# Kernel optimization log

Hardware: AMD Instinct MI355X
Metric: run time of the kernel (lower is better)

Reference implementation:

```python
import jax, jax.numpy as jnp
import numpy as np

Q = 10000   # num_question
D = 64      # dim_s
M = 50      # size_m
B = 64      # batch
T = 512     # seq_len


def setup_inputs() -> dict:
    key = jax.random.key(0)
    ks = jax.random.split(key, 14)
    s = 1.0 / np.sqrt(D)
    inp = {
        "question": jax.random.randint(ks[0], (B, T), 0, Q, dtype=jnp.int32),
        "response": jax.random.randint(ks[1], (B, T), 0, 2, dtype=jnp.int32),
        "mask": jnp.ones((B, T), dtype=jnp.float32),
        "k_emb": jax.random.normal(ks[2], (Q, D), jnp.float32) * s,
        "v_emb": jax.random.normal(ks[3], (2 * Q, D), jnp.float32) * s,
        "Mk": jax.random.normal(ks[4], (M, D), jnp.float32) * np.sqrt(2.0 / D),
        "Mv0": jax.random.normal(ks[5], (M, D), jnp.float32) * np.sqrt(2.0 / D),
        "e_W": jax.random.normal(ks[6], (D, D), jnp.float32) * s,
        "e_b": jnp.zeros((D,), jnp.float32),
        "a_W": jax.random.normal(ks[7], (D, D), jnp.float32) * s,
        "a_b": jnp.zeros((D,), jnp.float32),
        "f_W": jax.random.normal(ks[8], (2 * D, D), jnp.float32) * (1.0 / np.sqrt(2 * D)),
        "f_b": jnp.zeros((D,), jnp.float32),
        "p_W": jax.random.normal(ks[9], (D, 1), jnp.float32) * s,
        "p_b": jnp.zeros((1,), jnp.float32),
    }
    return inp


def reference(question, response, mask, k_emb, v_emb, Mk, Mv0,
              e_W, e_b, a_W, a_b, f_W, f_b, p_W, p_b):
    num_q = k_emb.shape[0]
    bsz = question.shape[0]
    x = question + num_q * response                      # [B,T] combined ids
    k = k_emb[question]                                  # [B,T,D]
    v = v_emb[x]                                         # [B,T,D]
    w = jax.nn.softmax(k @ Mk.T, axis=-1)                # [B,T,M] read/write weights
    e = jax.nn.sigmoid(v @ e_W + e_b)                    # [B,T,D] erase
    a = jnp.tanh(v @ a_W + a_b)                          # [B,T,D] add

    def step(Mvt, inp):
        wt, et, at, mt = inp                             # [B,M],[B,D],[B,D],[B]
        Mvn = Mvt * (1.0 - wt[:, :, None] * et[:, None, :]) + wt[:, :, None] * at[:, None, :]
        Mvt = jnp.where(mt[:, None, None] == 1, Mvn, Mvt)
        return Mvt, Mvt

    Mv0b = jnp.broadcast_to(Mv0, (bsz,) + Mv0.shape)     # [B,M,D]
    xs = (jnp.swapaxes(w, 0, 1), jnp.swapaxes(e, 0, 1),
          jnp.swapaxes(a, 0, 1), mask.T)
    _, Mv_seq = jax.lax.scan(step, Mv0b, xs)             # [T,B,M,D] states after steps 0..T-1
    # read at step t (t>=1) uses state after step t-1
    Mv_read = jnp.swapaxes(Mv_seq[:-1], 0, 1)            # [B,T-1,M,D]
    read = jnp.einsum('btm,btmd->btd', w[:, 1:], Mv_read)
    f = jnp.tanh(jnp.concatenate([read, k[:, 1:]], axis=-1) @ f_W + f_b)
    p = (f @ p_W + p_b).squeeze(-1)                      # [B,T-1]
    return p
```

## Files before the change

### kernel.cpp

```cpp
#include <hip/hip_runtime.h>
#include <cstddef>

#define QN 10000
#define DD 64
#define MM 50
#define BB 64
#define TT 512
#define WPAD 52
#define MG 25

__global__ __launch_bounds__(256) void kPre(
    const int* __restrict__ question, const int* __restrict__ response,
    const float* __restrict__ mask,
    const float* __restrict__ k_emb, const float* __restrict__ v_emb,
    const float* __restrict__ Mk,
    const float* __restrict__ e_W, const float* __restrict__ e_b,
    const float* __restrict__ a_W, const float* __restrict__ a_b,
    float* __restrict__ w_buf, float* __restrict__ e_buf,
    float* __restrict__ a_buf) {
  const int lane = (int)(threadIdx.x & 63);
  const int wslot = __builtin_amdgcn_readfirstlane((int)(threadIdx.x >> 6));
  const int gw = blockIdx.x * 4 + wslot;
  const int NW = gridDim.x * 4;
  const int third = NW / 3;
  if (gw >= 3 * third) return;
  const int role = gw / third;
  const int idx = gw - role * third;
  const int stride4 = third * 4;

  if (role == 0) {
    float mk[64];
    const int mrow = lane < MM ? lane : (MM - 1);
#pragma unroll
    for (int i = 0; i < 64; i += 4) {
      const float4 t4 = *(const float4*)(Mk + mrow * 64 + i);
      mk[i] = t4.x; mk[i + 1] = t4.y; mk[i + 2] = t4.z; mk[i + 3] = t4.w;
    }
    for (int base = idx * 4; base < BB * TT; base += stride4) {
      const int4 q4 = *(const int4*)(question + base);
      const float* __restrict__ kr0 = k_emb + (size_t)q4.x * 64;
      const float* __restrict__ kr1 = k_emb + (size_t)q4.y * 64;
      const float* __restrict__ kr2 = k_emb + (size_t)q4.z * 64;
      const float* __restrict__ kr3 = k_emb + (size_t)q4.w * 64;
      float l00=0.f,l01=0.f,l02=0.f,l03=0.f;
      float l10=0.f,l11=0.f,l12=0.f,l13=0.f;
      float l20=0.f,l21=0.f,l22=0.f,l23=0.f;
      float l30=0.f,l31=0.f,l32=0.f,l33=0.f;
#pragma unroll
      for (int i = 0; i < 64; i += 4) {
        const float4 k0 = *(const float4*)(kr0 + i);
        const float4 k1 = *(const float4*)(kr1 + i);
        const float4 k2 = *(const float4*)(kr2 + i);
        const float4 k3 = *(const float4*)(kr3 + i);
        l00 = fmaf(k0.x, mk[i], l00); l01 = fmaf(k0.y, mk[i+1], l01);
        l02 = fmaf(k0.z, mk[i+2], l02); l03 = fmaf(k0.w, mk[i+3], l03);
        l10 = fmaf(k1.x, mk[i], l10); l11 = fmaf(k1.y, mk[i+1], l11);
        l12 = fmaf(k1.z, mk[i+2], l12); l13 = fmaf(k1.w, mk[i+3], l13);
        l20 = fmaf(k2.x, mk[i], l20); l21 = fmaf(k2.y, mk[i+1], l21);
        l22 = fmaf(k2.z, mk[i+2], l22); l23 = fmaf(k2.w, mk[i+3], l23);
        l30 = fmaf(k3.x, mk[i], l30); l31 = fmaf(k3.y, mk[i+1], l31);
        l32 = fmaf(k3.z, mk[i+2], l32); l33 = fmaf(k3.w, mk[i+3], l33);
      }
      float lm[4];
      lm[0] = (l00 + l01) + (l02 + l03);
      lm[1] = (l10 + l11) + (l12 + l13);
      lm[2] = (l20 + l21) + (l22 + l23);
      lm[3] = (l30 + l31) + (l32 + l33);
#pragma unroll
      for (int r = 0; r < 4; ++r) {
        float lv = (lane < MM) ? lm[r] : -3.4e38f;
#pragma unroll
        for (int off = 32; off > 0; off >>= 1) lv = fmaxf(lv, __shfl_xor(lv, off));
        float pe = (lane < MM) ? __expf(lm[r] - lv) : 0.f;
        float ss = pe;
#pragma unroll
        for (int off = 32; off > 0; off >>= 1) ss += __shfl_xor(ss, off);
        if (lane < MM) w_buf[(size_t)(base + r) * WPAD + lane] = pe / ss;
      }
    }
  } else if (role == 1) {
    float ew[64];
#pragma unroll
    for (int i = 0; i < 64; ++i) ew[i] = e_W[i * 64 + lane];
    const float eb = e_b[lane];
    for (int base = idx * 4; base < BB * TT; base += stride4) {
      const int4 q4 = *(const int4*)(question + base);
      const int4 r4 = *(const int4*)(response + base);
      const float4 m4 = *(const float4*)(mask + base);
      const float* __restrict__ v0 = v_emb + ((size_t)q4.x + (size_t)QN * r4.x) * 64;
      const float* __restrict__ v1 = v_emb + ((size_t)q4.y + (size_t)QN * r4.y) * 64;
      const float* __restrict__ v2 = v_emb + ((size_t)q4.z + (size_t)QN * r4.z) * 64;
      const float* __restrict__ v3 = v_emb + ((size_t)q4.w + (size_t)QN * r4.w) * 64;
      float e00 = eb, e01 = 0.f, e10 = eb, e11 = 0.f;
      float e20 = eb, e21 = 0.f, e30 = eb, e31 = 0.f;
#pragma unroll
      for (int i = 0; i < 64; i += 2) {
        const float2 a0 = *(const float2*)(v0 + i);
        const float2 a1 = *(const float2*)(v1 + i);
        const float2 a2 = *(const float2*)(v2 + i);
        const float2 a3 = *(const float2*)(v3 + i);
        e00 = fmaf(a0.x, ew[i], e00); e01 = fmaf(a0.y, ew[i+1], e01);
        e10 = fmaf(a1.x, ew[i], e10); e11 = fmaf(a1.y, ew[i+1], e11);
        e20 = fmaf(a2.x, ew[i], e20); e21 = fmaf(a2.y, ew[i+1], e21);
        e30 = fmaf(a3.x, ew[i], e30); e31 = fmaf(a3.y, ew[i+1], e31);
      }
      const float mf0 = (m4.x == 1.0f) ? 1.0f : 0.0f;
      const float mf1 = (m4.y == 1.0f) ? 1.0f : 0.0f;
      const float mf2 = (m4.z == 1.0f) ? 1.0f : 0.0f;
      const float mf3 = (m4.w == 1.0f) ? 1.0f : 0.0f;
      e_buf[(size_t)(base + 0) * 64 + lane] = mf0 / (1.f + __expf(-(e00 + e01)));
      e_buf[(size_t)(base + 1) * 64 + lane] = mf1 / (1.f + __expf(-(e10 + e11)));
      e_buf[(size_t)(base + 2) * 64 + lane] = mf2 / (1.f + __expf(-(e20 + e21)));
      e_buf[(size_t)(base + 3) * 64 + lane] = mf3 / (1.f + __expf(-(e30 + e31)));
    }
  } else {
    float aw[64];
#pragma unroll
    for (int i = 0; i < 64; ++i) aw[i] = a_W[i * 64 + lane];
    const float ab = a_b[lane];
    for (int base = idx * 4; base < BB * TT; base += stride4) {
      const int4 q4 = *(const int4*)(question + base);
      const int4 r4 = *(const int4*)(response + base);
      const float4 m4 = *(const float4*)(mask + base);
      const float* __restrict__ v0 = v_emb + ((size_t)q4.x + (size_t)QN * r4.x) * 64;
      const float* __restrict__ v1 = v_emb + ((size_t)q4.y + (size_t)QN * r4.y) * 64;
      const float* __restrict__ v2 = v_emb + ((size_t)q4.z + (size_t)QN * r4.z) * 64;
      const float* __restrict__ v3 = v_emb + ((size_t)q4.w + (size_t)QN * r4.w) * 64;
      float a00 = ab, a01 = 0.f, a10 = ab, a11 = 0.f;
      float a20 = ab, a21 = 0.f, a30 = ab, a31 = 0.f;
#pragma unroll
      for (int i = 0; i < 64; i += 2) {
        const float2 x0 = *(const float2*)(v0 + i);
        const float2 x1 = *(const float2*)(v1 + i);
        const float2 x2 = *(const float2*)(v2 + i);
        const float2 x3 = *(const float2*)(v3 + i);
        a00 = fmaf(x0.x, aw[i], a00); a01 = fmaf(x0.y, aw[i+1], a01);
        a10 = fmaf(x1.x, aw[i], a10); a11 = fmaf(x1.y, aw[i+1], a11);
        a20 = fmaf(x2.x, aw[i], a20); a21 = fmaf(x2.y, aw[i+1], a21);
        a30 = fmaf(x3.x, aw[i], a30); a31 = fmaf(x3.y, aw[i+1], a31);
      }
      const float mf0 = (m4.x == 1.0f) ? 1.0f : 0.0f;
      const float mf1 = (m4.y == 1.0f) ? 1.0f : 0.0f;
      const float mf2 = (m4.z == 1.0f) ? 1.0f : 0.0f;
      const float mf3 = (m4.w == 1.0f) ? 1.0f : 0.0f;
      const float s0 = a00 + a01, s1 = a10 + a11, s2 = a20 + a21, s3 = a30 + a31;
      a_buf[(size_t)(base + 0) * 64 + lane] = mf0 * (1.f - 2.f / (__expf(2.f * s0) + 1.f));
      a_buf[(size_t)(base + 1) * 64 + lane] = mf1 * (1.f - 2.f / (__expf(2.f * s1) + 1.f));
      a_buf[(size_t)(base + 2) * 64 + lane] = mf2 * (1.f - 2.f / (__expf(2.f * s2) + 1.f));
      a_buf[(size_t)(base + 3) * 64 + lane] = mf3 * (1.f - 2.f / (__expf(2.f * s3) + 1.f));
    }
  }
}

__global__ __launch_bounds__(256) void kA16(
    const float* __restrict__ w_buf, const float* __restrict__ e_buf,
    const float* __restrict__ a_buf, float* __restrict__ AB) {
  const int lane = (int)(threadIdx.x & 63);
  const int wslot = __builtin_amdgcn_readfirstlane((int)(threadIdx.x >> 6));
  const int u2 = blockIdx.x * 4 + wslot;
  if (u2 >= BB * 32 * 2) return;
  const int g = u2 & 1;
  const int unit = u2 >> 1;
  const int b = unit >> 5;
  const int c = unit & 31;
  const size_t rowbase = (size_t)b * TT + c * 16;
  const size_t eb0 = rowbase * 64 + lane;

  float ev[16], av[16];
#pragma unroll
  for (int j = 0; j < 16; ++j) {
    ev[j] = e_buf[eb0 + (size_t)j * 64];
    av[j] = a_buf[eb0 + (size_t)j * 64];
  }

  float Am[MG], Bm[MG];
#pragma unroll
  for (int m = 0; m < MG; ++m) { Am[m] = 1.f; Bm[m] = 0.f; }

#pragma unroll
  for (int j = 0; j < 16; ++j) {
    const float* __restrict__ wr = w_buf + (rowbase + j) * WPAD + g * MG;
#pragma unroll
    for (int m = 0; m < MG; ++m) {
      const float wm = wr[m];
      const float al = fmaf(-wm, ev[j], 1.0f);
      const float be = wm * av[j];
      Am[m] *= al;
      Bm[m] = fmaf(Bm[m], al, be);
    }
  }
  float* __restrict__ abp = AB + (size_t)unit * 6400 + (g * MG) * 128 + lane * 2;
#pragma unroll
  for (int m = 0; m < MG; ++m) {
    float2 o; o.x = Am[m]; o.y = Bm[m];
    *(float2*)(abp + m * 128) = o;
  }
}

__global__ __launch_bounds__(256) void kB_entry(
    const float* __restrict__ AB, const float* __restrict__ Mv0,
    float* __restrict__ entry, int C) {
  const int NT = gridDim.x * 256;
  for (int idx = blockIdx.x * 256 + (int)threadIdx.x; idx < BB * MM * 64;
       idx += NT) {
    const int b = idx / (MM * 64);
    const int r = idx - b * (MM * 64);
    float s = Mv0[r];
    const float* __restrict__ abp = AB + (size_t)b * C * 6400 + (size_t)r * 2;
    float* __restrict__ ep = entry + (size_t)b * C * 3200 + r;
    if (C == 32) {
      float2 ab[32];
#pragma unroll
      for (int c = 0; c < 32; ++c)
        ab[c] = *(const float2*)(abp + (size_t)c * 6400);
#pragma unroll
      for (int c = 0; c < 32; ++c) {
        ep[(size_t)c * 3200] = s;
        s = fmaf(ab[c].x, s, ab[c].y);
      }
    } else {
      float2 cur = *(const float2*)(abp);
      for (int c = 0; c < C; ++c) {
        ep[(size_t)c * 3200] = s;
        float2 nxt; nxt.x = 1.f; nxt.y = 0.f;
        if (c + 1 < C) nxt = *(const float2*)(abp + (size_t)(c + 1) * 6400);
        s = fmaf(cur.x, s, cur.y);
        cur = nxt;
      }
    }
  }
}

__global__ __launch_bounds__(256) void kC16(
    const float* __restrict__ w_buf, const float* __restrict__ e_buf,
    const float* __restrict__ a_buf, const float* __restrict__ entry,
    float* __restrict__ read2) {
  const int lane = (int)(threadIdx.x & 63);
  const int wslot = __builtin_amdgcn_readfirstlane((int)(threadIdx.x >> 6));
  const int u2 = blockIdx.x * 4 + wslot;
  if (u2 >= BB * 32 * 2) return;
  const int g = u2 & 1;
  const int unit = u2 >> 1;
  const int b = unit >> 5;
  const int c = unit & 31;
  const size_t RN = (size_t)BB * (TT - 1) * 64;
  const size_t rowbase = (size_t)b * TT + c * 16;
  const size_t eb0 = rowbase * 64 + lane;

  float ev[16], av[16];
#pragma unroll
  for (int j = 0; j < 16; ++j) {
    ev[j] = e_buf[eb0 + (size_t)j * 64];
    av[j] = a_buf[eb0 + (size_t)j * 64];
  }

  float s[MG];
  {
    const float* __restrict__ ep =
        entry + (size_t)unit * 3200 + (g * MG) * 64 + lane;
#pragma unroll
    for (int m = 0; m < MG; ++m) s[m] = ep[m * 64];
  }

  const int t0 = c * 16;
  float* __restrict__ rb = read2 + (size_t)g * RN;
#pragma unroll
  for (int j = 0; j < 16; ++j) {
    const int t = t0 + j;
    const float* __restrict__ wr = w_buf + (rowbase + j) * WPAD + g * MG;
    if (t >= 1) {
      float a0 = 0.f, a1 = 0.f;
#pragma unroll
      for (int m = 0; m < MG - 1; m += 2) {
        a0 = fmaf(wr[m], s[m], a0);
        a1 = fmaf(wr[m + 1], s[m + 1], a1);
      }
      a0 = fmaf(wr[MG - 1], s[MG - 1], a0);
      rb[((size_t)b * (TT - 1) + (t - 1)) * 64 + lane] = a0 + a1;
    }
#pragma unroll
    for (int m = 0; m < MG; ++m)
      s[m] = fmaf(wr[m], fmaf(-s[m], ev[j], av[j]), s[m]);
  }
}

__global__ __launch_bounds__(256) void kA_chunk(
    const float* __restrict__ w_buf, const float* __restrict__ e_buf,
    const float* __restrict__ a_buf, float* __restrict__ AB, int logC, int L) {
  const int lane = (int)(threadIdx.x & 63);
  const int wslot = __builtin_amdgcn_readfirstlane((int)(threadIdx.x >> 6));
  const int NW = gridDim.x * 4;
  const int C = 1 << logC;
  for (int u2 = blockIdx.x * 4 + wslot; u2 < BB * C * 2; u2 += NW) {
    const int g = u2 & 1;
    const int unit = u2 >> 1;
    const int b = unit >> logC;
    const int c = unit & (C - 1);
    float Am[MG], Bm[MG];
#pragma unroll
    for (int m = 0; m < MG; ++m) { Am[m] = 1.f; Bm[m] = 0.f; }
    const size_t rowbase = (size_t)b * TT + c * L;
#pragma unroll 2
    for (int j = 0; j < L; ++j) {
      const size_t row = rowbase + j;
      const float ed = e_buf[row * 64 + lane];
      const float ad = a_buf[row * 64 + lane];
      const float* __restrict__ wr = w_buf + row * WPAD + g * MG;
#pragma unroll
      for (int m = 0; m < MG; ++m) {
        const float wm = wr[m];
        const float al = fmaf(-wm, ed, 1.0f);
        const float be = wm * ad;
        Am[m] *= al;
        Bm[m] = fmaf(Bm[m], al, be);
      }
    }
    float* __restrict__ abp = AB + (size_t)unit * 6400 + (g * MG) * 128 + lane * 2;
#pragma unroll
    for (int m = 0; m < MG; ++m) {
      float2 o; o.x = Am[m]; o.y = Bm[m];
      *(float2*)(abp + m * 128) = o;
    }
  }
}

__global__ __launch_bounds__(256) void kC_read(
    const float* __restrict__ w_buf, const float* __restrict__ e_buf,
    const float* __restrict__ a_buf, const float* __restrict__ entry,
    const float* __restrict__ Mv0, float* __restrict__ read2,
    int logC, int L, int use_mv0) {
  const int lane = (int)(threadIdx.x & 63);
  const int wslot = __builtin_amdgcn_readfirstlane((int)(threadIdx.x >> 6));
  const int NW = gridDim.x * 4;
  const int C = 1 << logC;
  const size_t RN = (size_t)BB * (TT - 1) * 64;
  for (int u2 = blockIdx.x * 4 + wslot; u2 < BB * C * 2; u2 += NW) {
    const int g = u2 & 1;
    const int unit = u2 >> 1;
    const int b = unit >> logC;
    const int c = unit & (C - 1);
    float s[MG];
    if (use_mv0) {
#pragma unroll
      for (int m = 0; m < MG; ++m) s[m] = Mv0[(g * MG + m) * 64 + lane];
    } else {
      const float* __restrict__ ep =
          entry + (size_t)unit * 3200 + (g * MG) * 64 + lane;
#pragma unroll
      for (int m = 0; m < MG; ++m) s[m] = ep[m * 64];
    }
    const int t0 = c * L;
    float* __restrict__ rb = read2 + (size_t)g * RN;
    for (int j = 0; j < L; ++j) {
      const int t = t0 + j;
      const size_t row = (size_t)b * TT + t;
      const float ed = e_buf[row * 64 + lane];
      const float ad = a_buf[row * 64 + lane];
      const float* __restrict__ wr = w_buf + row * WPAD + g * MG;
      if (t >= 1) {
        float a0 = 0.f, a1 = 0.f;
#pragma unroll
        for (int m = 0; m < MG - 1; m += 2) {
          a0 = fmaf(wr[m], s[m], a0);
          a1 = fmaf(wr[m + 1], s[m + 1], a1);
        }
        a0 = fmaf(wr[MG - 1], s[MG - 1], a0);
        rb[((size_t)b * (TT - 1) + (t - 1)) * 64 + lane] = a0 + a1;
      }
#pragma unroll
      for (int m = 0; m < MG; ++m)
        s[m] = fmaf(wr[m], fmaf(-s[m], ed, ad), s[m]);
    }
  }
}

__global__ __launch_bounds__(256) void k3_out(
    const int* __restrict__ question, const float* __restrict__ k_emb,
    const float* __restrict__ read2,
    const float* __restrict__ f_W, const float* __restrict__ f_b,
    const float* __restrict__ p_W, const float* __restrict__ p_b,
    float* __restrict__ out) {
  const int lane = (int)(threadIdx.x & 63);
  const int wslot = __builtin_amdgcn_readfirstlane((int)(threadIdx.x >> 6));
  const int NW = gridDim.x * 4;
  const size_t RN = (size_t)BB * (TT - 1) * 64;

  float fw[128];
#pragma unroll
  for (int i = 0; i < 128; ++i) fw[i] = f_W[i * 64 + lane];
  const float fb = f_b[lane];
  const float pw = p_W[lane];
  const float pb = p_b[0];

  for (int row = blockIdx.x * 4 + wslot; row < BB * (TT - 1); row += NW) {
    const int b = row / (TT - 1);
    const int tp = row - b * (TT - 1);
    const float* __restrict__ r0 = read2 + (size_t)row * 64;
    const float* __restrict__ r1 = r0 + RN;
    const int qn = question[b * TT + tp + 1];
    const float* __restrict__ krow = k_emb + (size_t)qn * 64;

    float f0 = fb, f1 = 0.f, f2 = 0.f, f3 = 0.f;
#pragma unroll
    for (int i = 0; i < 64; i += 4) {
      const float4 x0 = *(const float4*)(r0 + i);
      const float4 x1 = *(const float4*)(r1 + i);
      f0 = fmaf(x0.x + x1.x, fw[i], f0);
      f1 = fmaf(x0.y + x1.y, fw[i + 1], f1);
      f2 = fmaf(x0.z + x1.z, fw[i + 2], f2);
      f3 = fmaf(x0.w + x1.w, fw[i + 3], f3);
    }
#pragma unroll
    for (int i = 0; i < 64; i += 4) {
      const float4 kv = *(const float4*)(krow + i);
      f0 = fmaf(kv.x, fw[64 + i], f0);
      f1 = fmaf(kv.y, fw[64 + i + 1], f1);
      f2 = fmaf(kv.z, fw[64 + i + 2], f2);
      f3 = fmaf(kv.w, fw[64 + i + 3], f3);
    }
    const float f = (f0 + f1) + (f2 + f3);
    const float t2 = __expf(2.f * f);
    const float fv = 1.f - 2.f / (t2 + 1.f);
    float acc = fv * pw;
#pragma unroll
    for (int off = 32; off > 0; off >>= 1) acc += __shfl_xor(acc, off);
    if (lane == 0) out[row] = acc + pb;
  }
}

extern "C" void kernel_launch(void* const* d_in, const int* in_sizes, int n_in,
                              void* d_out, int out_size, void* d_ws, size_t ws_size,
                              hipStream_t stream) {
  const int*   question = (const int*)d_in[0];
  const int*   response = (const int*)d_in[1];
  const float* mask     = (const float*)d_in[2];
  const float* k_emb    = (const float*)d_in[3];
  const float* v_emb    = (const float*)d_in[4];
  const float* Mk       = (const float*)d_in[5];
  const float* Mv0      = (const float*)d_in[6];
  const float* e_W      = (const float*)d_in[7];
  const float* e_b      = (const float*)d_in[8];
  const float* a_W      = (const float*)d_in[9];
  const float* a_b      = (const float*)d_in[10];
  const float* f_W      = (const float*)d_in[11];
  const float* f_b      = (const float*)d_in[12];
  const float* p_W      = (const float*)d_in[13];
  const float* p_b      = (const float*)d_in[14];
  float* out = (float*)d_out;

  const size_t wN  = (size_t)BB * TT * WPAD;
  const size_t eN  = (size_t)BB * TT * 64;
  const size_t r2N = 2ull * BB * (TT - 1) * 64;
  float* ws = (float*)d_ws;
  float* w_buf  = ws;
  float* e_buf  = w_buf + wN;
  float* a_buf  = e_buf + eN;
  float* read2  = a_buf + eN;
  float* AB_arr = read2 + r2N;
  const size_t baseN = wN + 2 * eN + r2N;

  int C = 32, logC = 5;
  while (C >= 2) {
    const size_t need = (baseN + 9600ull * BB * C) * sizeof(float);
    if (need <= ws_size) break;
    C >>= 1; logC -= 1;
  }
  int useChunks = (C >= 2);
  if (!useChunks) { C = 1; logC = 0; }
  const int L = TT / C;
  float* entry = AB_arr + 6400ull * BB * C;

  hipLaunchKernelGGL(kPre, dim3(2048), dim3(256), 0, stream,
                     question, response, mask, k_emb, v_emb, Mk,
                     e_W, e_b, a_W, a_b, w_buf, e_buf, a_buf);

  if (C == 32) {
    hipLaunchKernelGGL(kA16, dim3(1024), dim3(256), 0, stream,
                       w_buf, e_buf, a_buf, AB_arr);
    hipLaunchKernelGGL(kB_entry, dim3((BB * MM * 64 + 255) / 256), dim3(256),
                       0, stream, AB_arr, Mv0, entry, C);
    hipLaunchKernelGGL(kC16, dim3(1024), dim3(256), 0, stream,
                       w_buf, e_buf, a_buf, entry, read2);
  } else {
    if (useChunks) {
      const int ublocksA = (BB * C * 2 + 3) / 4;
      hipLaunchKernelGGL(kA_chunk, dim3(ublocksA), dim3(256), 0, stream,
                         w_buf, e_buf, a_buf, AB_arr, logC, L);
      hipLaunchKernelGGL(kB_entry, dim3((BB * MM * 64 + 255) / 256), dim3(256),
                         0, stream, AB_arr, Mv0, entry, C);
    }
    const int ublocksC = (BB * C * 2 + 3) / 4;
    hipLaunchKernelGGL(kC_read, dim3(ublocksC), dim3(256), 0, stream,
                       w_buf, e_buf, a_buf, entry, Mv0, read2,
                       logC, L, useChunks ? 0 : 1);
  }

  hipLaunchKernelGGL(k3_out, dim3(1024), dim3(256), 0, stream,
                     question, k_emb, read2, f_W, f_b, p_W, p_b, out);
}
```

Measured before the change: 211.4 us.

## Fuse preprocessing with chunk scan and read with output projection

Replaces the five-kernel chunked-scan pipeline with three kernels. kPreA computes w/e/a for one 16-step chunk per block and builds the chunk's affine transfer coefficients from LDS. kCD replays each chunk from its entry state and feeds the read vectors straight into the f/p projection through LDS, so the read2 intermediate never goes through global memory. This saves two launches and a large round trip of intermediates, but per-block parallelism drops (192- and 128-thread blocks with heavy register use) and the fallback kPre path was rewritten to one row per wave.

```diff
diff --git a/kernel.cpp b/kernel.cpp
--- a/kernel.cpp
+++ b/kernel.cpp
@@ -8,6 +8,318 @@
 #define TT 512
 #define WPAD 52
 #define MG 25
+
+
+__global__ __attribute__((amdgpu_waves_per_eu(1, 2))) __launch_bounds__(192)
+void kPreA(
+    const int* __restrict__ question, const int* __restrict__ response,
+    const float* __restrict__ mask,
+    const float* __restrict__ k_emb, const float* __restrict__ v_emb,
+    const float* __restrict__ Mk,
+    const float* __restrict__ e_W, const float* __restrict__ e_b,
+    const float* __restrict__ a_W, const float* __restrict__ a_b,
+    float* __restrict__ w_buf, float* __restrict__ e_buf,
+    float* __restrict__ a_buf, float* __restrict__ AB) {
+  __shared__ float w_lds[16][52];
+  __shared__ float e_lds[16][64];
+  __shared__ float a_lds[16][64];
+  const int lane = (int)(threadIdx.x & 63);
+  const int wslot = __builtin_amdgcn_readfirstlane((int)(threadIdx.x >> 6));
+  const int unit = blockIdx.x;
+  const int b = unit >> 5;
+  const int c = unit & 31;
+  const size_t rowbase = (size_t)b * TT + c * 16;
+
+  if (wslot == 0) {
+    float mk[64];
+    const int mrow = lane < MM ? lane : (MM - 1);
+#pragma unroll
+    for (int i = 0; i < 64; i += 4) {
+      const float4 t4 = *(const float4*)(Mk + mrow * 64 + i);
+      mk[i] = t4.x; mk[i + 1] = t4.y; mk[i + 2] = t4.z; mk[i + 3] = t4.w;
+    }
+#pragma unroll
+    for (int base = 0; base < 16; base += 4) {
+      const int4 q4 = *(const int4*)(question + rowbase + base);
+      const float* __restrict__ kr0 = k_emb + (size_t)q4.x * 64;
+      const float* __restrict__ kr1 = k_emb + (size_t)q4.y * 64;
+      const float* __restrict__ kr2 = k_emb + (size_t)q4.z * 64;
+      const float* __restrict__ kr3 = k_emb + (size_t)q4.w * 64;
+      float l00=0.f,l01=0.f,l02=0.f,l03=0.f;
+      float l10=0.f,l11=0.f,l12=0.f,l13=0.f;
+      float l20=0.f,l21=0.f,l22=0.f,l23=0.f;
+      float l30=0.f,l31=0.f,l32=0.f,l33=0.f;
+#pragma unroll
+      for (int i = 0; i < 64; i += 4) {
+        const float4 k0 = *(const float4*)(kr0 + i);
+        const float4 k1 = *(const float4*)(kr1 + i);
+        const float4 k2 = *(const float4*)(kr2 + i);
+        const float4 k3 = *(const float4*)(kr3 + i);
+        l00 = fmaf(k0.x, mk[i], l00); l01 = fmaf(k0.y, mk[i+1], l01);
+        l02 = fmaf(k0.z, mk[i+2], l02); l03 = fmaf(k0.w, mk[i+3], l03);
+        l10 = fmaf(k1.x, mk[i], l10); l11 = fmaf(k1.y, mk[i+1], l11);
+        l12 = fmaf(k1.z, mk[i+2], l12); l13 = fmaf(k1.w, mk[i+3], l13);
+        l20 = fmaf(k2.x, mk[i], l20); l21 = fmaf(k2.y, mk[i+1], l21);
+        l22 = fmaf(k2.z, mk[i+2], l22); l23 = fmaf(k2.w, mk[i+3], l23);
+        l30 = fmaf(k3.x, mk[i], l30); l31 = fmaf(k3.y, mk[i+1], l31);
+        l32 = fmaf(k3.z, mk[i+2], l32); l33 = fmaf(k3.w, mk[i+3], l33);
+      }
+      float lm[4];
+      lm[0] = (l00 + l01) + (l02 + l03);
+      lm[1] = (l10 + l11) + (l12 + l13);
+      lm[2] = (l20 + l21) + (l22 + l23);
+      lm[3] = (l30 + l31) + (l32 + l33);
+#pragma unroll
+      for (int r = 0; r < 4; ++r) {
+        float lv = (lane < MM) ? lm[r] : -3.4e38f;
+#pragma unroll
+        for (int off = 32; off > 0; off >>= 1) lv = fmaxf(lv, __shfl_xor(lv, off));
+        float pe = (lane < MM) ? __expf(lm[r] - lv) : 0.f;
+        float ss = pe;
+#pragma unroll
+        for (int off = 32; off > 0; off >>= 1) ss += __shfl_xor(ss, off);
+        if (lane < MM) {
+          const float wv = pe / ss;
+          w_buf[(rowbase + base + r) * WPAD + lane] = wv;
+          w_lds[base + r][lane] = wv;
+        }
+      }
+    }
+  } else if (wslot == 1) {
+    float ew[64];
+#pragma unroll
+    for (int i = 0; i < 64; ++i) ew[i] = e_W[i * 64 + lane];
+    const float eb = e_b[lane];
+#pragma unroll
+    for (int base = 0; base < 16; base += 4) {
+      const int4 q4 = *(const int4*)(question + rowbase + base);
+      const int4 r4 = *(const int4*)(response + rowbase + base);
+      const float4 m4 = *(const float4*)(mask + rowbase + base);
+      const float* __restrict__ v0 = v_emb + ((size_t)q4.x + (size_t)QN * r4.x) * 64;
+      const float* __restrict__ v1 = v_emb + ((size_t)q4.y + (size_t)QN * r4.y) * 64;
+      const float* __restrict__ v2 = v_emb + ((size_t)q4.z + (size_t)QN * r4.z) * 64;
+      const float* __restrict__ v3 = v_emb + ((size_t)q4.w + (size_t)QN * r4.w) * 64;
+      float e00 = eb, e01 = 0.f, e10 = eb, e11 = 0.f;
+      float e20 = eb, e21 = 0.f, e30 = eb, e31 = 0.f;
+#pragma unroll
+      for (int i = 0; i < 64; i += 2) {
+        const float2 a0 = *(const float2*)(v0 + i);
+        const float2 a1 = *(const float2*)(v1 + i);
+        const float2 a2 = *(const float2*)(v2 + i);
+        const float2 a3 = *(const float2*)(v3 + i);
+        e00 = fmaf(a0.x, ew[i], e00); e01 = fmaf(a0.y, ew[i+1], e01);
+        e10 = fmaf(a1.x, ew[i], e10); e11 = fmaf(a1.y, ew[i+1], e11);
+        e20 = fmaf(a2.x, ew[i], e20); e21 = fmaf(a2.y, ew[i+1], e21);
+        e30 = fmaf(a3.x, ew[i], e30); e31 = fmaf(a3.y, ew[i+1], e31);
+      }
+      const float mf0 = (m4.x == 1.0f) ? 1.0f : 0.0f;
+      const float mf1 = (m4.y == 1.0f) ? 1.0f : 0.0f;
+      const float mf2 = (m4.z == 1.0f) ? 1.0f : 0.0f;
+      const float mf3 = (m4.w == 1.0f) ? 1.0f : 0.0f;
+      const float o0 = mf0 / (1.f + __expf(-(e00 + e01)));
+      const float o1 = mf1 / (1.f + __expf(-(e10 + e11)));
+      const float o2 = mf2 / (1.f + __expf(-(e20 + e21)));
+      const float o3 = mf3 / (1.f + __expf(-(e30 + e31)));
+      e_buf[(rowbase + base + 0) * 64 + lane] = o0; e_lds[base + 0][lane] = o0;
+      e_buf[(rowbase + base + 1) * 64 + lane] = o1; e_lds[base + 1][lane] = o1;
+      e_buf[(rowbase + base + 2) * 64 + lane] = o2; e_lds[base + 2][lane] = o2;
+      e_buf[(rowbase + base + 3) * 64 + lane] = o3; e_lds[base + 3][lane] = o3;
+    }
+  } else {
+    float aw[64];
+#pragma unroll
+    for (int i = 0; i < 64; ++i) aw[i] = a_W[i * 64 + lane];
+    const float ab = a_b[lane];
+#pragma unroll
+    for (int base = 0; base < 16; base += 4) {
+      const int4 q4 = *(const int4*)(question + rowbase + base);
+      const int4 r4 = *(const int4*)(response + rowbase + base);
+      const float4 m4 = *(const float4*)(mask + rowbase + base);
+      const float* __restrict__ v0 = v_emb + ((size_t)q4.x + (size_t)QN * r4.x) * 64;
+      const float* __restrict__ v1 = v_emb + ((size_t)q4.y + (size_t)QN * r4.y) * 64;
+      const float* __restrict__ v2 = v_emb + ((size_t)q4.z + (size_t)QN * r4.z) * 64;
+      const float* __restrict__ v3 = v_emb + ((size_t)q4.w + (size_t)QN * r4.w) * 64;
+      float a00 = ab, a01 = 0.f, a10 = ab, a11 = 0.f;
+      float a20 = ab, a21 = 0.f, a30 = ab, a31 = 0.f;
+#pragma unroll
+      for (int i = 0; i < 64; i += 2) {
+        const float2 x0 = *(const float2*)(v0 + i);
+        const float2 x1 = *(const float2*)(v1 + i);
+        const float2 x2 = *(const float2*)(v2 + i);
+        const float2 x3 = *(const float2*)(v3 + i);
+        a00 = fmaf(x0.x, aw[i], a00); a01 = fmaf(x0.y, aw[i+1], a01);
+        a10 = fmaf(x1.x, aw[i], a10); a11 = fmaf(x1.y, aw[i+1], a11);
+        a20 = fmaf(x2.x, aw[i], a20); a21 = fmaf(x2.y, aw[i+1], a21);
+        a30 = fmaf(x3.x, aw[i], a30); a31 = fmaf(x3.y, aw[i+1], a31);
+      }
+      const float mf0 = (m4.x == 1.0f) ? 1.0f : 0.0f;
+      const float mf1 = (m4.y == 1.0f) ? 1.0f : 0.0f;
+      const float mf2 = (m4.z == 1.0f) ? 1.0f : 0.0f;
+      const float mf3 = (m4.w == 1.0f) ? 1.0f : 0.0f;
+      const float s0 = a00 + a01, s1 = a10 + a11, s2 = a20 + a21, s3 = a30 + a31;
+      const float o0 = mf0 * (1.f - 2.f / (__expf(2.f * s0) + 1.f));
+      const float o1 = mf1 * (1.f - 2.f / (__expf(2.f * s1) + 1.f));
+      const float o2 = mf2 * (1.f - 2.f / (__expf(2.f * s2) + 1.f));
+      const float o3 = mf3 * (1.f - 2.f / (__expf(2.f * s3) + 1.f));
+      a_buf[(rowbase + base + 0) * 64 + lane] = o0; a_lds[base + 0][lane] = o0;
+      a_buf[(rowbase + base + 1) * 64 + lane] = o1; a_lds[base + 1][lane] = o1;
+      a_buf[(rowbase + base + 2) * 64 + lane] = o2; a_lds[base + 2][lane] = o2;
+      a_buf[(rowbase + base + 3) * 64 + lane] = o3; a_lds[base + 3][lane] = o3;
+    }
+  }
+  __syncthreads();
+
+  if (wslot < 2) {
+    const int g = wslot;
+    float Am[MG], Bm[MG];
+#pragma unroll
+    for (int m = 0; m < MG; ++m) { Am[m] = 1.f; Bm[m] = 0.f; }
+#pragma unroll
+    for (int j = 0; j < 16; ++j) {
+      const float ed = e_lds[j][lane];
+      const float ad = a_lds[j][lane];
+#pragma unroll
+      for (int m = 0; m < MG; ++m) {
+        const float wm = w_lds[j][g * MG + m];
+        const float al = fmaf(-wm, ed, 1.0f);
+        const float be = wm * ad;
+        Am[m] *= al;
+        Bm[m] = fmaf(Bm[m], al, be);
+      }
+    }
+    float* __restrict__ abp = AB + (size_t)unit * 6400 + (g * MG) * 128 + lane * 2;
+#pragma unroll
+    for (int m = 0; m < MG; ++m) {
+      float2 o; o.x = Am[m]; o.y = Bm[m];
+      *(float2*)(abp + m * 128) = o;
+    }
+  }
+}
+
+__global__ __launch_bounds__(256) void kB_entry(
+    const float* __restrict__ AB, const float* __restrict__ Mv0,
+    float* __restrict__ entry, int C) {
+  const int NT = gridDim.x * 256;
+  for (int idx = blockIdx.x * 256 + (int)threadIdx.x; idx < BB * MM * 64;
+       idx += NT) {
+    const int b = idx / (MM * 64);
+    const int r = idx - b * (MM * 64);
+    float s = Mv0[r];
+    const float* __restrict__ abp = AB + (size_t)b * C * 6400 + (size_t)r * 2;
+    float* __restrict__ ep = entry + (size_t)b * C * 3200 + r;
+    if (C == 32) {
+      float2 ab[32];
+#pragma unroll
+      for (int c = 0; c < 32; ++c)
+        ab[c] = *(const float2*)(abp + (size_t)c * 6400);
+#pragma unroll
+      for (int c = 0; c < 32; ++c) {
+        ep[(size_t)c * 3200] = s;
+        s = fmaf(ab[c].x, s, ab[c].y);
+      }
+    } else {
+      float2 cur = *(const float2*)(abp);
+      for (int c = 0; c < C; ++c) {
+        ep[(size_t)c * 3200] = s;
+        float2 nxt; nxt.x = 1.f; nxt.y = 0.f;
+        if (c + 1 < C) nxt = *(const float2*)(abp + (size_t)(c + 1) * 6400);
+        s = fmaf(cur.x, s, cur.y);
+        cur = nxt;
+      }
+    }
+  }
+}
+
+__global__ __attribute__((amdgpu_waves_per_eu(1, 2))) __launch_bounds__(128)
+void kCD(
+    const int* __restrict__ question,
+    const float* __restrict__ w_buf, const float* __restrict__ e_buf,
+    const float* __restrict__ a_buf, const float* __restrict__ entry,
+    const float* __restrict__ k_emb,
+    const float* __restrict__ f_W, const float* __restrict__ f_b,
+    const float* __restrict__ p_W, const float* __restrict__ p_b,
+    float* __restrict__ out) {
+  __shared__ float p_lds[2][16][64];
+  const int lane = (int)(threadIdx.x & 63);
+  const int g = __builtin_amdgcn_readfirstlane((int)(threadIdx.x >> 6));
+  const int unit = blockIdx.x;
+  const int b = unit >> 5;
+  const int c = unit & 31;
+  const size_t rowbase = (size_t)b * TT + c * 16;
+  const size_t eb0 = rowbase * 64 + lane;
+
+  {
+    float ev[16], av[16];
+#pragma unroll
+    for (int j = 0; j < 16; ++j) {
+      ev[j] = e_buf[eb0 + (size_t)j * 64];
+      av[j] = a_buf[eb0 + (size_t)j * 64];
+    }
+    float s[MG];
+    const float* __restrict__ ep =
+        entry + (size_t)unit * 3200 + (g * MG) * 64 + lane;
+#pragma unroll
+    for (int m = 0; m < MG; ++m) s[m] = ep[m * 64];
+
+#pragma unroll
+    for (int j = 0; j < 16; ++j) {
+      const float* __restrict__ wr = w_buf + (rowbase + j) * WPAD + g * MG;
+      float a0 = 0.f, a1 = 0.f;
+#pragma unroll
+      for (int m = 0; m < MG - 1; m += 2) {
+        a0 = fmaf(wr[m], s[m], a0);
+        a1 = fmaf(wr[m + 1], s[m + 1], a1);
+      }
+      a0 = fmaf(wr[MG - 1], s[MG - 1], a0);
+      p_lds[g][j][lane] = a0 + a1;
+#pragma unroll
+      for (int m = 0; m < MG; ++m)
+        s[m] = fmaf(wr[m], fmaf(-s[m], ev[j], av[j]), s[m]);
+    }
+  }
+  __syncthreads();
+
+  float fw[128];
+#pragma unroll
+  for (int i = 0; i < 128; ++i) fw[i] = f_W[i * 64 + lane];
+  const float fb = f_b[lane];
+  const float pw = p_W[lane];
+  const float pb = p_b[0];
+
+  int j0 = g * 8;
+  const int j1 = j0 + 8;
+  if (c == 0 && g == 0) j0 = 1;
+  for (int j = j0; j < j1; ++j) {
+    const int t = c * 16 + j;
+    const int qn = question[(size_t)b * TT + t];
+    const float* __restrict__ krow = k_emb + (size_t)qn * 64;
+    float f0 = fb, f1 = 0.f, f2 = 0.f, f3 = 0.f;
+#pragma unroll
+    for (int i = 0; i < 64; i += 4) {
+      const float4 x0 = *(const float4*)(&p_lds[0][j][i]);
+      const float4 x1 = *(const float4*)(&p_lds[1][j][i]);
+      f0 = fmaf(x0.x + x1.x, fw[i], f0);
+      f1 = fmaf(x0.y + x1.y, fw[i + 1], f1);
+      f2 = fmaf(x0.z + x1.z, fw[i + 2], f2);
+      f3 = fmaf(x0.w + x1.w, fw[i + 3], f3);
+    }
+#pragma unroll
+    for (int i = 0; i < 64; i += 4) {
+      const float4 kv = *(const float4*)(krow + i);
+      f0 = fmaf(kv.x, fw[64 + i], f0);
+      f1 = fmaf(kv.y, fw[64 + i + 1], f1);
+      f2 = fmaf(kv.z, fw[64 + i + 2], f2);
+      f3 = fmaf(kv.w, fw[64 + i + 3], f3);
+    }
+    const float fsum = (f0 + f1) + (f2 + f3);
+    const float t2 = __expf(2.f * fsum);
+    const float fv = 1.f - 2.f / (t2 + 1.f);
+    float acc = fv * pw;
+#pragma unroll
+    for (int off = 32; off > 0; off >>= 1) acc += __shfl_xor(acc, off);
+    if (lane == 0) out[(size_t)b * (TT - 1) + (t - 1)] = acc + pb;
+  }
+}
 
 __global__ __launch_bounds__(256) void kPre(
     const int* __restrict__ question, const int* __restrict__ response,
@@ -26,7 +338,6 @@
   if (gw >= 3 * third) return;
   const int role = gw / third;
   const int idx = gw - role * third;
-  const int stride4 = third * 4;
 
   if (role == 0) {
     float mk[64];
@@ -36,251 +347,67 @@
       const float4 t4 = *(const float4*)(Mk + mrow * 64 + i);
       mk[i] = t4.x; mk[i + 1] = t4.y; mk[i + 2] = t4.z; mk[i + 3] = t4.w;
     }
-    for (int base = idx * 4; base < BB * TT; base += stride4) {
-      const int4 q4 = *(const int4*)(question + base);
-      const float* __restrict__ kr0 = k_emb + (size_t)q4.x * 64;
-      const float* __restrict__ kr1 = k_emb + (size_t)q4.y * 64;
-      const float* __restrict__ kr2 = k_emb + (size_t)q4.z * 64;
-      const float* __restrict__ kr3 = k_emb + (size_t)q4.w * 64;
-      float l00=0.f,l01=0.f,l02=0.f,l03=0.f;
-      float l10=0.f,l11=0.f,l12=0.f,l13=0.f;
-      float l20=0.f,l21=0.f,l22=0.f,l23=0.f;
-      float l30=0.f,l31=0.f,l32=0.f,l33=0.f;
+    for (int row = idx; row < BB * TT; row += third) {
+      const int q = question[row];
+      const float* __restrict__ krow = k_emb + (size_t)q * 64;
+      float l0 = 0.f, l1 = 0.f, l2 = 0.f, l3 = 0.f;
 #pragma unroll
       for (int i = 0; i < 64; i += 4) {
-        const float4 k0 = *(const float4*)(kr0 + i);
-        const float4 k1 = *(const float4*)(kr1 + i);
-        const float4 k2 = *(const float4*)(kr2 + i);
-        const float4 k3 = *(const float4*)(kr3 + i);
-        l00 = fmaf(k0.x, mk[i], l00); l01 = fmaf(k0.y, mk[i+1], l01);
-        l02 = fmaf(k0.z, mk[i+2], l02); l03 = fmaf(k0.w, mk[i+3], l03);
-        l10 = fmaf(k1.x, mk[i], l10); l11 = fmaf(k1.y, mk[i+1], l11);
-        l12 = fmaf(k1.z, mk[i+2], l12); l13 = fmaf(k1.w, mk[i+3], l13);
-        l20 = fmaf(k2.x, mk[i], l20); l21 = fmaf(k2.y, mk[i+1], l21);
-        l22 = fmaf(k2.z, mk[i+2], l22); l23 = fmaf(k2.w, mk[i+3], l23);
-        l30 = fmaf(k3.x, mk[i], l30); l31 = fmaf(k3.y, mk[i+1], l31);
-        l32 = fmaf(k3.z, mk[i+2], l32); l33 = fmaf(k3.w, mk[i+3], l33);
-      }
-      float lm[4];
-      lm[0] = (l00 + l01) + (l02 + l03);
-      lm[1] = (l10 + l11) + (l12 + l13);
-      lm[2] = (l20 + l21) + (l22 + l23);
-      lm[3] = (l30 + l31) + (l32 + l33);
-#pragma unroll
-      for (int r = 0; r < 4; ++r) {
-        float lv = (lane < MM) ? lm[r] : -3.4e38f;
-#pragma unroll
-        for (int off = 32; off > 0; off >>= 1) lv = fmaxf(lv, __shfl_xor(lv, off));
-        float pe = (lane < MM) ? __expf(lm[r] - lv) : 0.f;
-        float ss = pe;
-#pragma unroll
-        for (int off = 32; off > 0; off >>= 1) ss += __shfl_xor(ss, off);
-        if (lane < MM) w_buf[(size_t)(base + r) * WPAD + lane] = pe / ss;
-      }
+        const float4 kv = *(const float4*)(krow + i);
+        l0 = fmaf(kv.x, mk[i], l0);
+        l1 = fmaf(kv.y, mk[i + 1], l1);
+        l2 = fmaf(kv.z, mk[i + 2], l2);
+        l3 = fmaf(kv.w, mk[i + 3], l3);
+      }
+      const float lm = (l0 + l1) + (l2 + l3);
+      float lv = (lane < MM) ? lm : -3.4e38f;
+#pragma unroll
+      for (int off = 32; off > 0; off >>= 1) lv = fmaxf(lv, __shfl_xor(lv, off));
+      float pe = (lane < MM) ? __expf(lm - lv) : 0.f;
+      float ss = pe;
+#pragma unroll
+      for (int off = 32; off > 0; off >>= 1) ss += __shfl_xor(ss, off);
+      if (lane < MM) w_buf[(size_t)row * WPAD + lane] = pe / ss;
     }
   } else if (role == 1) {
     float ew[64];
 #pragma unroll
     for (int i = 0; i < 64; ++i) ew[i] = e_W[i * 64 + lane];
     const float eb = e_b[lane];
-    for (int base = idx * 4; base < BB * TT; base += stride4) {
-      const int4 q4 = *(const int4*)(question + base);
-      const int4 r4 = *(const int4*)(response + base);
-      const float4 m4 = *(const float4*)(mask + base);
-      const float* __restrict__ v0 = v_emb + ((size_t)q4.x + (size_t)QN * r4.x) * 64;
-      const float* __restrict__ v1 = v_emb + ((size_t)q4.y + (size_t)QN * r4.y) * 64;
-      const float* __restrict__ v2 = v_emb + ((size_t)q4.z + (size_t)QN * r4.z) * 64;
-      const float* __restrict__ v3 = v_emb + ((size_t)q4.w + (size_t)QN * r4.w) * 64;
-      float e00 = eb, e01 = 0.f, e10 = eb, e11 = 0.f;
-      float e20 = eb, e21 = 0.f, e30 = eb, e31 = 0.f;
+    for (int row = idx; row < BB * TT; row += third) {
+      const int q = question[row];
+      const int r = response[row];
+      const float mf = (mask[row] == 1.0f) ? 1.0f : 0.0f;
+      const float* __restrict__ vrow = v_emb + ((size_t)q + (size_t)QN * r) * 64;
+      float e0 = eb, e1 = 0.f;
 #pragma unroll
       for (int i = 0; i < 64; i += 2) {
-        const float2 a0 = *(const float2*)(v0 + i);
-        const float2 a1 = *(const float2*)(v1 + i);
-        const float2 a2 = *(const float2*)(v2 + i);
-        const float2 a3 = *(const float2*)(v3 + i);
-        e00 = fmaf(a0.x, ew[i], e00); e01 = fmaf(a0.y, ew[i+1], e01);
-        e10 = fmaf(a1.x, ew[i], e10); e11 = fmaf(a1.y, ew[i+1], e11);
-        e20 = fmaf(a2.x, ew[i], e20); e21 = fmaf(a2.y, ew[i+1], e21);
-        e30 = fmaf(a3.x, ew[i], e30); e31 = fmaf(a3.y, ew[i+1], e31);
-      }
-      const float mf0 = (m4.x == 1.0f) ? 1.0f : 0.0f;
-      const float mf1 = (m4.y == 1.0f) ? 1.0f : 0.0f;
-      const float mf2 = (m4.z == 1.0f) ? 1.0f : 0.0f;
-      const float mf3 = (m4.w == 1.0f) ? 1.0f : 0.0f;
-      e_buf[(size_t)(base + 0) * 64 + lane] = mf0 / (1.f + __expf(-(e00 + e01)));
-      e_buf[(size_t)(base + 1) * 64 + lane] = mf1 / (1.f + __expf(-(e10 + e11)));
-      e_buf[(size_t)(base + 2) * 64 + lane] = mf2 / (1.f + __expf(-(e20 + e21)));
-      e_buf[(size_t)(base + 3) * 64 + lane] = mf3 / (1.f + __expf(-(e30 + e31)));
+        const float2 vv = *(const float2*)(vrow + i);
+        e0 = fmaf(vv.x, ew[i], e0);
+        e1 = fmaf(vv.y, ew[i + 1], e1);
+      }
+      e_buf[(size_t)row * 64 + lane] = mf / (1.f + __expf(-(e0 + e1)));
     }
   } else {
     float aw[64];
 #pragma unroll
     for (int i = 0; i < 64; ++i) aw[i] = a_W[i * 64 + lane];
     const float ab = a_b[lane];
-    for (int base = idx * 4; base < BB * TT; base += stride4) {
-      const int4 q4 = *(const int4*)(question + base);
-      const int4 r4 = *(const int4*)(response + base);
-      const float4 m4 = *(const float4*)(mask + base);
-      const float* __restrict__ v0 = v_emb + ((size_t)q4.x + (size_t)QN * r4.x) * 64;
-      const float* __restrict__ v1 = v_emb + ((size_t)q4.y + (size_t)QN * r4.y) * 64;
-      const float* __restrict__ v2 = v_emb + ((size_t)q4.z + (size_t)QN * r4.z) * 64;
-      const float* __restrict__ v3 = v_emb + ((size_t)q4.w + (size_t)QN * r4.w) * 64;
-      float a00 = ab, a01 = 0.f, a10 = ab, a11 = 0.f;
-      float a20 = ab, a21 = 0.f, a30 = ab, a31 = 0.f;
+    for (int row = idx; row < BB * TT; row += third) {
+      const int q = question[row];
+      const int r = response[row];
+      const float mf = (mask[row] == 1.0f) ? 1.0f : 0.0f;
+      const float* __restrict__ vrow = v_emb + ((size_t)q + (size_t)QN * r) * 64;
+      float a0 = ab, a1 = 0.f;
 #pragma unroll
       for (int i = 0; i < 64; i += 2) {
-        const float2 x0 = *(const float2*)(v0 + i);
-        const float2 x1 = *(const float2*)(v1 + i);
-        const float2 x2 = *(const float2*)(v2 + i);
-        const float2 x3 = *(const float2*)(v3 + i);
-        a00 = fmaf(x0.x, aw[i], a00); a01 = fmaf(x0.y, aw[i+1], a01);
-        a10 = fmaf(x1.x, aw[i], a10); a11 = fmaf(x1.y, aw[i+1], a11);
-        a20 = fmaf(x2.x, aw[i], a20); a21 = fmaf(x2.y, aw[i+1], a21);
-        a30 = fmaf(x3.x, aw[i], a30); a31 = fmaf(x3.y, aw[i+1], a31);
-      }
-      const float mf0 = (m4.x == 1.0f) ? 1.0f : 0.0f;
-      const float mf1 = (m4.y == 1.0f) ? 1.0f : 0.0f;
-      const float mf2 = (m4.z == 1.0f) ? 1.0f : 0.0f;
-      const float mf3 = (m4.w == 1.0f) ? 1.0f : 0.0f;
-      const float s0 = a00 + a01, s1 = a10 + a11, s2 = a20 + a21, s3 = a30 + a31;
-      a_buf[(size_t)(base + 0) * 64 + lane] = mf0 * (1.f - 2.f / (__expf(2.f * s0) + 1.f));
-      a_buf[(size_t)(base + 1) * 64 + lane] = mf1 * (1.f - 2.f / (__expf(2.f * s1) + 1.f));
-      a_buf[(size_t)(base + 2) * 64 + lane] = mf2 * (1.f - 2.f / (__expf(2.f * s2) + 1.f));
-      a_buf[(size_t)(base + 3) * 64 + lane] = mf3 * (1.f - 2.f / (__expf(2.f * s3) + 1.f));
-    }
-  }
-}
-
-__global__ __launch_bounds__(256) void kA16(
-    const float* __restrict__ w_buf, const float* __restrict__ e_buf,
-    const float* __restrict__ a_buf, float* __restrict__ AB) {
-  const int lane = (int)(threadIdx.x & 63);
-  const int wslot = __builtin_amdgcn_readfirstlane((int)(threadIdx.x >> 6));
-  const int u2 = blockIdx.x * 4 + wslot;
-  if (u2 >= BB * 32 * 2) return;
-  const int g = u2 & 1;
-  const int unit = u2 >> 1;
-  const int b = unit >> 5;
-  const int c = unit & 31;
-  const size_t rowbase = (size_t)b * TT + c * 16;
-  const size_t eb0 = rowbase * 64 + lane;
-
-  float ev[16], av[16];
-#pragma unroll
-  for (int j = 0; j < 16; ++j) {
-    ev[j] = e_buf[eb0 + (size_t)j * 64];
-    av[j] = a_buf[eb0 + (size_t)j * 64];
-  }
-
-  float Am[MG], Bm[MG];
-#pragma unroll
-  for (int m = 0; m < MG; ++m) { Am[m] = 1.f; Bm[m] = 0.f; }
-
-#pragma unroll
-  for (int j = 0; j < 16; ++j) {
-    const float* __restrict__ wr = w_buf + (rowbase + j) * WPAD + g * MG;
-#pragma unroll
-    for (int m = 0; m < MG; ++m) {
-      const float wm = wr[m];
-      const float al = fmaf(-wm, ev[j], 1.0f);
-      const float be = wm * av[j];
-      Am[m] *= al;
-      Bm[m] = fmaf(Bm[m], al, be);
-    }
-  }
-  float* __restrict__ abp = AB + (size_t)unit * 6400 + (g * MG) * 128 + lane * 2;
-#pragma unroll
-  for (int m = 0; m < MG; ++m) {
-    float2 o; o.x = Am[m]; o.y = Bm[m];
-    *(float2*)(abp + m * 128) = o;
-  }
-}
-
-__global__ __launch_bounds__(256) void kB_entry(
-    const float* __restrict__ AB, const float* __restrict__ Mv0,
-    float* __restrict__ entry, int C) {
-  const int NT = gridDim.x * 256;
-  for (int idx = blockIdx.x * 256 + (int)threadIdx.x; idx < BB * MM * 64;
-       idx += NT) {
-    const int b = idx / (MM * 64);
-    const int r = idx - b * (MM * 64);
-    float s = Mv0[r];
-    const float* __restrict__ abp = AB + (size_t)b * C * 6400 + (size_t)r * 2;
-    float* __restrict__ ep = entry + (size_t)b * C * 3200 + r;
-    if (C == 32) {
-      float2 ab[32];
-#pragma unroll
-      for (int c = 0; c < 32; ++c)
-        ab[c] = *(const float2*)(abp + (size_t)c * 6400);
-#pragma unroll
-      for (int c = 0; c < 32; ++c) {
-        ep[(size_t)c * 3200] = s;
-        s = fmaf(ab[c].x, s, ab[c].y);
-      }
-    } else {
-      float2 cur = *(const float2*)(abp);
-      for (int c = 0; c < C; ++c) {
-        ep[(size_t)c * 3200] = s;
-        float2 nxt; nxt.x = 1.f; nxt.y = 0.f;
-        if (c + 1 < C) nxt = *(const float2*)(abp + (size_t)(c + 1) * 6400);
-        s = fmaf(cur.x, s, cur.y);
-        cur = nxt;
-      }
-    }
-  }
-}
-
-__global__ __launch_bounds__(256) void kC16(
-    const float* __restrict__ w_buf, const float* __restrict__ e_buf,
-    const float* __restrict__ a_buf, const float* __restrict__ entry,
-    float* __restrict__ read2) {
-  const int lane = (int)(threadIdx.x & 63);
-  const int wslot = __builtin_amdgcn_readfirstlane((int)(threadIdx.x >> 6));
-  const int u2 = blockIdx.x * 4 + wslot;
-  if (u2 >= BB * 32 * 2) return;
-  const int g = u2 & 1;
-  const int unit = u2 >> 1;
-  const int b = unit >> 5;
-  const int c = unit & 31;
-  const size_t RN = (size_t)BB * (TT - 1) * 64;
-  const size_t rowbase = (size_t)b * TT + c * 16;
-  const size_t eb0 = rowbase * 64 + lane;
-
-  float ev[16], av[16];
-#pragma unroll
-  for (int j = 0; j < 16; ++j) {
-    ev[j] = e_buf[eb0 + (size_t)j * 64];
-    av[j] = a_buf[eb0 + (size_t)j * 64];
-  }
-
-  float s[MG];
-  {
-    const float* __restrict__ ep =
-        entry + (size_t)unit * 3200 + (g * MG) * 64 + lane;
-#pragma unroll
-    for (int m = 0; m < MG; ++m) s[m] = ep[m * 64];
-  }
-
-  const int t0 = c * 16;
-  float* __restrict__ rb = read2 + (size_t)g * RN;
-#pragma unroll
-  for (int j = 0; j < 16; ++j) {
-    const int t = t0 + j;
-    const float* __restrict__ wr = w_buf + (rowbase + j) * WPAD + g * MG;
-    if (t >= 1) {
-      float a0 = 0.f, a1 = 0.f;
-#pragma unroll
-      for (int m = 0; m < MG - 1; m += 2) {
-        a0 = fmaf(wr[m], s[m], a0);
-        a1 = fmaf(wr[m + 1], s[m + 1], a1);
-      }
-      a0 = fmaf(wr[MG - 1], s[MG - 1], a0);
-      rb[((size_t)b * (TT - 1) + (t - 1)) * 64 + lane] = a0 + a1;
-    }
-#pragma unroll
-    for (int m = 0; m < MG; ++m)
-      s[m] = fmaf(wr[m], fmaf(-s[m], ev[j], av[j]), s[m]);
+        const float2 vv = *(const float2*)(vrow + i);
+        a0 = fmaf(vv.x, aw[i], a0);
+        a1 = fmaf(vv.y, aw[i + 1], a1);
+      }
+      const float sa = a0 + a1;
+      a_buf[(size_t)row * 64 + lane] = mf * (1.f - 2.f / (__expf(2.f * sa) + 1.f));
+    }
   }
 }
 
@@ -374,7 +501,8 @@
   }
 }
 
-__global__ __launch_bounds__(256) void k3_out(
+__global__ __attribute__((amdgpu_waves_per_eu(1, 2))) __launch_bounds__(256)
+void k3_out(
     const int* __restrict__ question, const float* __restrict__ k_emb,
     const float* __restrict__ read2,
     const float* __restrict__ f_W, const float* __restrict__ f_b,
@@ -448,17 +576,32 @@
   const float* p_b      = (const float*)d_in[14];
   float* out = (float*)d_out;
 
-  const size_t wN  = (size_t)BB * TT * WPAD;
-  const size_t eN  = (size_t)BB * TT * 64;
+  const size_t wN = (size_t)BB * TT * WPAD;
+  const size_t eN = (size_t)BB * TT * 64;
+  float* ws = (float*)d_ws;
+  float* w_buf = ws;
+  float* e_buf = w_buf + wN;
+  float* a_buf = e_buf + eN;
+
+  const size_t mainNeed = (wN + 2 * eN + 9600ull * BB * 32) * sizeof(float);
+  if (mainNeed <= ws_size) {
+    float* AB_arr = a_buf + eN;
+    float* entry  = AB_arr + 6400ull * BB * 32;
+    hipLaunchKernelGGL(kPreA, dim3(BB * 32), dim3(192), 0, stream,
+                       question, response, mask, k_emb, v_emb, Mk,
+                       e_W, e_b, a_W, a_b, w_buf, e_buf, a_buf, AB_arr);
+    hipLaunchKernelGGL(kB_entry, dim3((BB * MM * 64 + 255) / 256), dim3(256),
+                       0, stream, AB_arr, Mv0, entry, 32);
+    hipLaunchKernelGGL(kCD, dim3(BB * 32), dim3(128), 0, stream,
+                       question, w_buf, e_buf, a_buf, entry, k_emb,
+                       f_W, f_b, p_W, p_b, out);
+    return;
+  }
+
   const size_t r2N = 2ull * BB * (TT - 1) * 64;
-  float* ws = (float*)d_ws;
-  float* w_buf  = ws;
-  float* e_buf  = w_buf + wN;
-  float* a_buf  = e_buf + eN;
   float* read2  = a_buf + eN;
   float* AB_arr = read2 + r2N;
   const size_t baseN = wN + 2 * eN + r2N;
-
   int C = 32, logC = 5;
   while (C >= 2) {
     const size_t need = (baseN + 9600ull * BB * C) * sizeof(float);
@@ -473,28 +616,17 @@
   hipLaunchKernelGGL(kPre, dim3(2048), dim3(256), 0, stream,
                      question, response, mask, k_emb, v_emb, Mk,
                      e_W, e_b, a_W, a_b, w_buf, e_buf, a_buf);
-
-  if (C == 32) {
-    hipLaunchKernelGGL(kA16, dim3(1024), dim3(256), 0, stream,
-                       w_buf, e_buf, a_buf, AB_arr);
+  if (useChunks) {
+    const int ublocksA = (BB * C * 2 + 3) / 4;
+    hipLaunchKernelGGL(kA_chunk, dim3(ublocksA), dim3(256), 0, stream,
+                       w_buf, e_buf, a_buf, AB_arr, logC, L);
     hipLaunchKernelGGL(kB_entry, dim3((BB * MM * 64 + 255) / 256), dim3(256),
                        0, stream, AB_arr, Mv0, entry, C);
-    hipLaunchKernelGGL(kC16, dim3(1024), dim3(256), 0, stream,
-                       w_buf, e_buf, a_buf, entry, read2);
-  } else {
-    if (useChunks) {
-      const int ublocksA = (BB * C * 2 + 3) / 4;
-      hipLaunchKernelGGL(kA_chunk, dim3(ublocksA), dim3(256), 0, stream,
-                         w_buf, e_buf, a_buf, AB_arr, logC, L);
-      hipLaunchKernelGGL(kB_entry, dim3((BB * MM * 64 + 255) / 256), dim3(256),
-                         0, stream, AB_arr, Mv0, entry, C);
-    }
-    const int ublocksC = (BB * C * 2 + 3) / 4;
-    hipLaunchKernelGGL(kC_read, dim3(ublocksC), dim3(256), 0, stream,
-                       w_buf, e_buf, a_buf, entry, Mv0, read2,
-                       logC, L, useChunks ? 0 : 1);
-  }
-
+  }
+  const int ublocksC = (BB * C * 2 + 3) / 4;
+  hipLaunchKernelGGL(kC_read, dim3(ublocksC), dim3(256), 0, stream,
+                     w_buf, e_buf, a_buf, entry, Mv0, read2,
+                     logC, L, useChunks ? 0 : 1);
   hipLaunchKernelGGL(k3_out, dim3(1024), dim3(256), 0, stream,
                      question, k_emb, read2, f_W, f_b, p_W, p_b, out);
 }
```

New measurement: 243.8 us. 15.3% more time.
